# Kernel tuning notes

Measured on AMD Instinct MI355X. Metric: run time of the kernel, lower is better.

The kernel has to match this reference:

```python
import jax, jax.numpy as jnp
import numpy as np

B, C, D_MODEL, N_HEADS = 2, 2048, 1024, 16


def rotary_matrix(context_length: int, d: int) -> jnp.ndarray:
    """Faithful vectorization of get_rotary_matrix: theta = 10000^(-2*(i-1)/d)."""
    half = d // 2
    i = jnp.arange(half, dtype=jnp.float32)
    theta = 10000.0 ** (-2.0 * (i - 1.0) / d)          # note the (i-1), as in source
    m = jnp.arange(context_length, dtype=jnp.float32)
    ang = m[:, None] * theta                            # [C, d/2]
    c, s = jnp.cos(ang), jnp.sin(ang)
    ev = 2 * jnp.arange(half)
    od = ev + 1
    R = jnp.zeros((context_length, d, d), jnp.float32)
    R = R.at[:, ev, ev].set(c)
    R = R.at[:, ev, od].set(-s)
    R = R.at[:, od, ev].set(s)
    R = R.at[:, od, od].set(c)
    return R


def setup_inputs() -> dict:
    key = jax.random.key(0)
    k1, k2, k3, k4 = jax.random.split(key, 4)
    x = jax.random.normal(k1, (B, C, D_MODEL), dtype=jnp.float32)
    w_qkv = jax.random.normal(k2, (3 * D_MODEL, D_MODEL), dtype=jnp.float32) * 0.02
    w_out = jax.random.normal(k3, (D_MODEL, D_MODEL), dtype=jnp.float32) * 0.02
    b_out = jax.random.normal(k4, (D_MODEL,), dtype=jnp.float32) * 0.02
    return {"x": x, "w_qkv": w_qkv, "w_out": w_out, "b_out": b_out}


def reference(x, w_qkv, w_out, b_out):
    b, c, d = x.shape
    h = N_HEADS
    dh = d // h
    qkv = x @ w_qkv.T                                   # [B,C,3D]
    q, k, v = jnp.split(qkv, 3, axis=-1)
    # [B,C,D] -> [B,H,C,dh]
    q = q.reshape(b, c, h, dh).transpose(0, 2, 1, 3)
    k = k.reshape(b, c, h, dh).transpose(0, 2, 1, 3)
    v = v.reshape(b, c, h, dh).transpose(0, 2, 1, 3)
    R = rotary_matrix(c, dh)                            # [C,dh,dh]
    q_rot = jnp.einsum('bhci,cij->bhcj', q, R)
    k_rot = jnp.einsum('bhci,cij->bhcj', k, R)
    scale = jnp.sqrt(jnp.float32(dh))
    # exact math of the source: exp with no max subtraction, separate num/den
    attn_num = jnp.exp(jnp.einsum('bhqd,bhkd->bhqk', q_rot, k_rot) / scale)
    attn_den = jnp.exp(jnp.einsum('bhqd,bhkd->bhqk', q, k) / scale)
    attn_den = jnp.sum(attn_den, axis=-1, keepdims=True)
    attn = attn_num / attn_den
    causal = jnp.tril(jnp.ones((c, c), jnp.float32))[None, None]
    attn = jnp.where(causal == 0, 0.0, attn)
    y = jnp.einsum('bhqk,bhkd->bhqd', attn, v)
    y = y.transpose(0, 2, 1, 3).reshape(b, c, d)
    return y @ w_out.T + b_out
```

## Files before the change

### kernel.cpp

```cpp
#include <hip/hip_runtime.h>
#include <math.h>
#include <stdint.h>

#define BB 2
#define CC 2048
#define DD 1024
#define HH 16
#define DHH 64
#define HALF 32

typedef __attribute__((ext_vector_type(8))) short bf16x8;
typedef __attribute__((ext_vector_type(4))) float f32x4;
typedef unsigned int u32;

#define EXPC 0.1803368801f

__device__ __forceinline__ ushort f2bf(float f) {
    uint32_t u = __builtin_bit_cast(uint32_t, f);
    u = (u + 0x7FFFu + ((u >> 16) & 1u)) >> 16;
    return (ushort)u;
}

__device__ __forceinline__ void gload16(const void* g, void* lds) {
    __builtin_amdgcn_global_load_lds(
        (const u32 __attribute__((address_space(1)))*)g,
        (u32 __attribute__((address_space(3)))*)lds, 16, 0, 0);
}

__global__ __launch_bounds__(256) void cast3_k(const float* __restrict__ x,
                                               const float* __restrict__ wq,
                                               const float* __restrict__ wo,
                                               ushort* __restrict__ xb,
                                               ushort* __restrict__ wqb,
                                               ushort* __restrict__ wob) {
    int id = blockIdx.x * 256 + threadIdx.x;
    const float* s;
    ushort* d;
    int off;
    if (id < 524288)       { s = x;  d = xb;  off = id; }
    else if (id < 917504)  { s = wq; d = wqb; off = id - 524288; }
    else                   { s = wo; d = wob; off = id - 917504; }
    float4 a = *reinterpret_cast<const float4*>(s + (size_t)off * 8);
    float4 b = *reinterpret_cast<const float4*>(s + (size_t)off * 8 + 4);
    bf16x8 o;
    o[0] = (short)f2bf(a.x); o[1] = (short)f2bf(a.y);
    o[2] = (short)f2bf(a.z); o[3] = (short)f2bf(a.w);
    o[4] = (short)f2bf(b.x); o[5] = (short)f2bf(b.y);
    o[6] = (short)f2bf(b.z); o[7] = (short)f2bf(b.w);
    *reinterpret_cast<bf16x8*>(d + (size_t)off * 8) = o;
}

__global__ __launch_bounds__(256) void rope_table_k(float* __restrict__ ct, float* __restrict__ st) {
    int idx = blockIdx.x * 256 + threadIdx.x;
    if (idx >= CC * HALF) return;
    int m = idx >> 5;
    int t = idx & 31;
    double theta_d = pow(10000.0, -2.0 * ((double)t - 1.0) / 64.0);
    float theta = (float)theta_d;
    float ang = (float)m * theta;
    ct[idx] = cosf(ang);
    st[idx] = sinf(ang);
}

__global__ __launch_bounds__(256) void qkv_gemm_mfma_k(const ushort* __restrict__ xb,
                                                       const ushort* __restrict__ wqb,
                                                       const float* __restrict__ ct,
                                                       const float* __restrict__ st,
                                                       ushort* __restrict__ q,
                                                       ushort* __restrict__ k,
                                                       ushort* __restrict__ qr,
                                                       ushort* __restrict__ kr,
                                                       ushort* __restrict__ vT3) {
    __shared__ ushort Al[128 * 64];
    __shared__ ushort Bl[128 * 64];
    const int tid = threadIdx.x;
    const int w = tid >> 6, l = tid & 63;
    const int l15 = l & 15, lg = l >> 4;
    const int wr = w >> 1, wc = w & 1;
    const int m0 = blockIdx.x * 128, n0 = blockIdx.y * 128;
    const int lrow = l >> 3, lch = l & 7;

    f32x4 acc[4][4];
#pragma unroll
    for (int i = 0; i < 4; i++)
#pragma unroll
        for (int j = 0; j < 4; j++) acc[i][j] = (f32x4){0.f, 0.f, 0.f, 0.f};

    for (int k0 = 0; k0 < 1024; k0 += 64) {
        __syncthreads();
#pragma unroll
        for (int c = 0; c < 4; c++) {
            int row = w * 32 + c * 8 + lrow;
            int gch = (lch ^ (row & 7)) * 8;
            gload16(xb + (size_t)(m0 + row) * 1024 + k0 + gch, &Al[(w * 32 + c * 8) * 64]);
            gload16(wqb + (size_t)(n0 + row) * 1024 + k0 + gch, &Bl[(w * 32 + c * 8) * 64]);
        }
        __syncthreads();
#pragma unroll
        for (int kk = 0; kk < 2; kk++) {
            bf16x8 a[4], b[4];
#pragma unroll
            for (int mt = 0; mt < 4; mt++) {
                int row = wr * 64 + mt * 16 + l15;
                a[mt] = *reinterpret_cast<const bf16x8*>(&Al[row * 64 + ((kk * 4 + lg) ^ (row & 7)) * 8]);
            }
#pragma unroll
            for (int nt = 0; nt < 4; nt++) {
                int row = wc * 64 + nt * 16 + l15;
                b[nt] = *reinterpret_cast<const bf16x8*>(&Bl[row * 64 + ((kk * 4 + lg) ^ (row & 7)) * 8]);
            }
#pragma unroll
            for (int mt = 0; mt < 4; mt++)
#pragma unroll
                for (int nt = 0; nt < 4; nt++)
                    acc[mt][nt] = __builtin_amdgcn_mfma_f32_16x16x32_bf16(a[mt], b[nt], acc[mt][nt], 0, 0, 0);
        }
    }
#pragma unroll
    for (int mt = 0; mt < 4; mt++)
#pragma unroll
        for (int nt = 0; nt < 4; nt++) {
            int n = n0 + wc * 64 + nt * 16 + l15;
            int part = n >> 10;
            int d = n & 1023;
            int h = d >> 6, dd = d & 63;
            int mbase = m0 + wr * 64 + mt * 16 + lg * 4;
            int bb = mbase >> 11, cpos = mbase & 2047;
            if (part == 2) {
                int kt = cpos >> 6, kcol = cpos & 63;
                ushort4 pk;
                pk.x = f2bf(acc[mt][nt][0]); pk.y = f2bf(acc[mt][nt][1]);
                pk.z = f2bf(acc[mt][nt][2]); pk.w = f2bf(acc[mt][nt][3]);
                size_t off = ((((size_t)(bb * HH + h)) * 32 + kt) * 64 + dd) * 64 + kcol;
                *reinterpret_cast<ushort4*>(vT3 + off) = pk;
            } else {
                ushort* dstu = (part == 0) ? q : k;
                ushort* dstr = (part == 0) ? qr : kr;
                const float sgn = (dd & 1) ? -1.f : 1.f;
                const int t = dd >> 1;
#pragma unroll
                for (int r = 0; r < 4; r++) {
                    float val = acc[mt][nt][r];
                    float par = __shfl_xor(val, 1, 64);
                    float c = ct[(cpos + r) * 32 + t];
                    float s = st[(cpos + r) * 32 + t];
                    float rot = val * c + sgn * par * s;
                    size_t base = (((size_t)bb * HH + h) * CC + (cpos + r)) * DHH + dd;
                    dstu[base] = f2bf(val);
                    dstr[base] = f2bf(rot);
                }
            }
        }
}

__global__ __launch_bounds__(256, 2) void attn_fused_k(const ushort* __restrict__ vT3,
                                                       const ushort* __restrict__ qg,
                                                       const ushort* __restrict__ kg,
                                                       const ushort* __restrict__ qrg,
                                                       const ushort* __restrict__ krg,
                                                       ushort* __restrict__ y) {
    __shared__ ushort Kl[2][64 * 64];
    __shared__ ushort Krl[2][64 * 64];
    __shared__ ushort Pl[4][16 * 64];

    const int tid = threadIdx.x;
    const int w = tid >> 6, l = tid & 63;
    const int l15 = l & 15, lg = l >> 4;
    const int lrow = l >> 3, lch = l & 7;

    const int bid = blockIdx.x;
    const int xcd = bid & 7;
    const int idx = bid >> 3;
    const int sub = idx & 3;
    const int tp = idx >> 2;
    const int bh = xcd * 4 + sub;
    const int NB = 31 - tp;
    const int q0a = tp * 64;
    const int q0b = NB * 64;

    const ushort* qb  = qg  + (size_t)bh * CC * DHH;
    const ushort* kb  = kg  + (size_t)bh * CC * DHH;
    const ushort* qrb = qrg + (size_t)bh * CC * DHH;
    const ushort* krb = krg + (size_t)bh * CC * DHH;
    const ushort* vtb = vT3 + (size_t)bh * 32 * 64 * 64;

    bf16x8 qfA[2], qfB[2], qrfA[2], qrfB[2];
#pragma unroll
    for (int kk = 0; kk < 2; kk++) {
        int ra = q0a + w * 16 + l15;
        int rb = q0b + w * 16 + l15;
        qfA[kk]  = *reinterpret_cast<const bf16x8*>(qb  + (size_t)ra * DHH + kk * 32 + lg * 8);
        qfB[kk]  = *reinterpret_cast<const bf16x8*>(qb  + (size_t)rb * DHH + kk * 32 + lg * 8);
        qrfA[kk] = *reinterpret_cast<const bf16x8*>(qrb + (size_t)ra * DHH + kk * 32 + lg * 8);
        qrfB[kk] = *reinterpret_cast<const bf16x8*>(qrb + (size_t)rb * DHH + kk * 32 + lg * 8);
    }

    f32x4 yaccA[4], yaccB[4];
#pragma unroll
    for (int nt = 0; nt < 4; nt++) {
        yaccA[nt] = (f32x4){0.f, 0.f, 0.f, 0.f};
        yaccB[nt] = (f32x4){0.f, 0.f, 0.f, 0.f};
    }
    float daccA0 = 0.f, daccA1 = 0.f, daccB0 = 0.f, daccB1 = 0.f;

#define STAGE(KT, BUF)                                                                         \
    {                                                                                          \
        const int sk0 = (KT) * 64;                                                             \
        _Pragma("unroll")                                                                      \
        for (int c = 0; c < 2; c++) {                                                          \
            int row = w * 16 + c * 8 + lrow;                                                   \
            int gch = (lch ^ (row & 7)) * 8;                                                   \
            gload16(kb + (size_t)(sk0 + row) * DHH + gch, &Kl[BUF][(w * 16 + c * 8) * 64]);    \
            if ((KT) <= NB)                                                                    \
                gload16(krb + (size_t)(sk0 + row) * DHH + gch, &Krl[BUF][(w * 16 + c * 8) * 64]); \
        }                                                                                      \
    }

#define NUMPV(Q0, QRF, YACC, LASTKT)                                                           \
    {                                                                                          \
        const bool diag = (kt == (LASTKT));                                                    \
        const int qrow = (Q0) + w * 16 + l15;                                                  \
        _Pragma("unroll")                                                                      \
        for (int nt = 0; nt < 4; nt++) {                                                       \
            bf16x8 kra0, kra1;                                                                 \
            {                                                                                  \
                int krow = nt * 16 + l15;                                                      \
                kra0 = *reinterpret_cast<const bf16x8*>(&Krl[cur][krow * 64 + ((0 + lg) ^ (krow & 7)) * 8]); \
                kra1 = *reinterpret_cast<const bf16x8*>(&Krl[cur][krow * 64 + ((4 + lg) ^ (krow & 7)) * 8]); \
            }                                                                                  \
            __builtin_amdgcn_s_setprio(1);                                                     \
            f32x4 s = (f32x4){0.f, 0.f, 0.f, 0.f};                                             \
            s = __builtin_amdgcn_mfma_f32_16x16x32_bf16(kra0, (QRF)[0], s, 0, 0, 0);           \
            s = __builtin_amdgcn_mfma_f32_16x16x32_bf16(kra1, (QRF)[1], s, 0, 0, 0);           \
            __builtin_amdgcn_s_setprio(0);                                                     \
            float pe[4];                                                                       \
            _Pragma("unroll")                                                                  \
            for (int r = 0; r < 4; r++)                                                        \
                pe[r] = __builtin_amdgcn_exp2f(s[r] * EXPC);                                   \
            if (diag) {                                                                        \
                _Pragma("unroll")                                                              \
                for (int r = 0; r < 4; r++) {                                                  \
                    int key = kt * 64 + nt * 16 + lg * 4 + r;                                  \
                    pe[r] = (key <= qrow) ? pe[r] : 0.f;                                       \
                }                                                                              \
            }                                                                                  \
            u32 pk0, pk1;                                                                      \
            asm("v_cvt_pk_bf16_f32 %0, %1, %2" : "=v"(pk0) : "v"(pe[0]), "v"(pe[1]));          \
            asm("v_cvt_pk_bf16_f32 %0, %1, %2" : "=v"(pk1) : "v"(pe[2]), "v"(pe[3]));          \
            int swzc = (nt * 2 + (lg >> 1)) ^ (l15 & 7);                                       \
            uint2 pr; pr.x = pk0; pr.y = pk1;                                                  \
            *reinterpret_cast<uint2*>(&Pl[w][l15 * 64 + swzc * 8 + (lg & 1) * 4]) = pr;        \
        }                                                                                      \
        bf16x8 pa[2];                                                                          \
        _Pragma("unroll")                                                                      \
        for (int kk2 = 0; kk2 < 2; kk2++) {                                                    \
            int rc = (kk2 * 4 + lg) ^ (l15 & 7);                                               \
            pa[kk2] = *reinterpret_cast<const bf16x8*>(&Pl[w][l15 * 64 + rc * 8]);             \
        }                                                                                      \
        __builtin_amdgcn_s_setprio(1);                                                         \
        _Pragma("unroll")                                                                      \
        for (int nt2 = 0; nt2 < 4; nt2++) {                                                    \
            (YACC)[nt2] = __builtin_amdgcn_mfma_f32_16x16x32_bf16(pa[0], vf[nt2][0], (YACC)[nt2], 0, 0, 0); \
            (YACC)[nt2] = __builtin_amdgcn_mfma_f32_16x16x32_bf16(pa[1], vf[nt2][1], (YACC)[nt2], 0, 0, 0); \
        }                                                                                      \
        __builtin_amdgcn_s_setprio(0);                                                         \
    }

    STAGE(0, 0);
    __syncthreads();
    int cur = 0;

    for (int kt = 0; kt < 32; kt++) {
        const bool actA = (kt <= tp);
        const bool actB = (kt <= NB);

        bf16x8 vf[4][2];
        if (actB) {
            const ushort* vt0 = vtb + (size_t)kt * 64 * 64;
#pragma unroll
            for (int nt2 = 0; nt2 < 4; nt2++)
#pragma unroll
                for (int kk2 = 0; kk2 < 2; kk2++)
                    vf[nt2][kk2] = *reinterpret_cast<const bf16x8*>(
                        vt0 + (nt2 * 16 + l15) * 64 + kk2 * 32 + lg * 8);
        }

        if (kt + 1 < 32) STAGE(kt + 1, cur ^ 1);

#pragma unroll
        for (int nt = 0; nt < 4; nt++) {
            bf16x8 ka0, ka1;
            {
                int krow = nt * 16 + l15;
                ka0 = *reinterpret_cast<const bf16x8*>(&Kl[cur][krow * 64 + ((0 + lg) ^ (krow & 7)) * 8]);
                ka1 = *reinterpret_cast<const bf16x8*>(&Kl[cur][krow * 64 + ((4 + lg) ^ (krow & 7)) * 8]);
            }
            __builtin_amdgcn_s_setprio(1);
            f32x4 sA = (f32x4){0.f, 0.f, 0.f, 0.f};
            sA = __builtin_amdgcn_mfma_f32_16x16x32_bf16(ka0, qfA[0], sA, 0, 0, 0);
            sA = __builtin_amdgcn_mfma_f32_16x16x32_bf16(ka1, qfA[1], sA, 0, 0, 0);
            f32x4 sB = (f32x4){0.f, 0.f, 0.f, 0.f};
            sB = __builtin_amdgcn_mfma_f32_16x16x32_bf16(ka0, qfB[0], sB, 0, 0, 0);
            sB = __builtin_amdgcn_mfma_f32_16x16x32_bf16(ka1, qfB[1], sB, 0, 0, 0);
            __builtin_amdgcn_s_setprio(0);
            if (nt & 1) {
#pragma unroll
                for (int r = 0; r < 4; r++) {
                    daccA1 += __builtin_amdgcn_exp2f(sA[r] * EXPC);
                    daccB1 += __builtin_amdgcn_exp2f(sB[r] * EXPC);
                }
            } else {
#pragma unroll
                for (int r = 0; r < 4; r++) {
                    daccA0 += __builtin_amdgcn_exp2f(sA[r] * EXPC);
                    daccB0 += __builtin_amdgcn_exp2f(sB[r] * EXPC);
                }
            }
        }

        if (actB) NUMPV(q0b, qrfB, yaccB, NB);
        if (actA) NUMPV(q0a, qrfA, yaccA, tp);

        __syncthreads();
        cur ^= 1;
    }

    float denA = daccA0 + daccA1, denB = daccB0 + daccB1;
    denA += __shfl_xor(denA, 16, 64);
    denA += __shfl_xor(denA, 32, 64);
    denB += __shfl_xor(denB, 16, 64);
    denB += __shfl_xor(denB, 32, 64);

    const int b = bh >> 4, h = bh & 15;
#pragma unroll
    for (int r = 0; r < 4; r++) {
        float drA = __shfl(denA, lg * 4 + r, 64);
        float drB = __shfl(denB, lg * 4 + r, 64);
        float invA = 1.f / drA;
        float invB = 1.f / drB;
        int rowA = q0a + w * 16 + lg * 4 + r;
        int rowB = q0b + w * 16 + lg * 4 + r;
#pragma unroll
        for (int nt2 = 0; nt2 < 4; nt2++) {
            y[((size_t)b * CC + rowA) * DD + h * DHH + nt2 * 16 + l15] = f2bf(yaccA[nt2][r] * invA);
            y[((size_t)b * CC + rowB) * DD + h * DHH + nt2 * 16 + l15] = f2bf(yaccB[nt2][r] * invB);
        }
    }
#undef STAGE
#undef NUMPV
}

__global__ __launch_bounds__(256) void out_proj_mfma_k(const ushort* __restrict__ yb,
                                                       const ushort* __restrict__ wob,
                                                       const float* __restrict__ bias,
                                                       float* __restrict__ out) {
    __shared__ ushort Al[128 * 64];
    __shared__ ushort Bl[128 * 64];
    const int tid = threadIdx.x;
    const int w = tid >> 6, l = tid & 63;
    const int l15 = l & 15, lg = l >> 4;
    const int wr = w >> 1, wc = w & 1;
    const int m0 = blockIdx.x * 128, n0 = blockIdx.y * 128;
    const int lrow = l >> 3, lch = l & 7;

    f32x4 acc[4][4];
#pragma unroll
    for (int i = 0; i < 4; i++)
#pragma unroll
        for (int j = 0; j < 4; j++) acc[i][j] = (f32x4){0.f, 0.f, 0.f, 0.f};

    for (int k0 = 0; k0 < 1024; k0 += 64) {
        __syncthreads();
#pragma unroll
        for (int c = 0; c < 4; c++) {
            int row = w * 32 + c * 8 + lrow;
            int gch = (lch ^ (row & 7)) * 8;
            gload16(yb + (size_t)(m0 + row) * 1024 + k0 + gch, &Al[(w * 32 + c * 8) * 64]);
            gload16(wob + (size_t)(n0 + row) * 1024 + k0 + gch, &Bl[(w * 32 + c * 8) * 64]);
        }
        __syncthreads();
#pragma unroll
        for (int kk = 0; kk < 2; kk++) {
            bf16x8 a[4], b[4];
#pragma unroll
            for (int mt = 0; mt < 4; mt++) {
                int row = wr * 64 + mt * 16 + l15;
                a[mt] = *reinterpret_cast<const bf16x8*>(&Al[row * 64 + ((kk * 4 + lg) ^ (row & 7)) * 8]);
            }
#pragma unroll
            for (int nt = 0; nt < 4; nt++) {
                int row = wc * 64 + nt * 16 + l15;
                b[nt] = *reinterpret_cast<const bf16x8*>(&Bl[row * 64 + ((kk * 4 + lg) ^ (row & 7)) * 8]);
            }
#pragma unroll
            for (int mt = 0; mt < 4; mt++)
#pragma unroll
                for (int nt = 0; nt < 4; nt++)
                    acc[mt][nt] = __builtin_amdgcn_mfma_f32_16x16x32_bf16(a[mt], b[nt], acc[mt][nt], 0, 0, 0);
        }
    }
#pragma unroll
    for (int mt = 0; mt < 4; mt++)
#pragma unroll
        for (int nt = 0; nt < 4; nt++) {
            int n = n0 + wc * 64 + nt * 16 + l15;
            float bv = bias[n];
#pragma unroll
            for (int r = 0; r < 4; r++) {
                int m = m0 + wr * 64 + mt * 16 + lg * 4 + r;
                out[(size_t)m * 1024 + n] = acc[mt][nt][r] + bv;
            }
        }
}

extern "C" void kernel_launch(void* const* d_in, const int* in_sizes, int n_in,
                              void* d_out, int out_size, void* d_ws, size_t ws_size,
                              hipStream_t stream) {
    (void)in_sizes; (void)n_in; (void)out_size; (void)ws_size;
    const float* x     = (const float*)d_in[0];
    const float* w_qkv = (const float*)d_in[1];
    const float* w_out = (const float*)d_in[2];
    const float* b_out = (const float*)d_in[3];
    float* out = (float*)d_out;

    char* p = (char*)d_ws;
    float* ct = (float*)p;  p += (size_t)CC * HALF * 4;
    float* st = (float*)p;  p += (size_t)CC * HALF * 4;
    ushort* xb  = (ushort*)p; p += (size_t)4096 * 1024 * 2;
    ushort* wqb = (ushort*)p; p += (size_t)3072 * 1024 * 2;
    ushort* wob = (ushort*)p; p += (size_t)1024 * 1024 * 2;
    const size_t TEN = (size_t)BB * HH * CC * DHH;
    ushort* qb = (ushort*)p; p += TEN * 2;
    ushort* kb = (ushort*)p; p += TEN * 2;
    ushort* vT = (ushort*)p; p += TEN * 2;
    ushort* qr = (ushort*)p; p += TEN * 2;
    ushort* kr = (ushort*)p; p += TEN * 2;
    ushort* yb = (ushort*)p; p += (size_t)4096 * 1024 * 2;

    cast3_k<<<dim3(4096), dim3(256), 0, stream>>>(x, w_qkv, w_out, xb, wqb, wob);
    rope_table_k<<<dim3((CC * HALF) / 256), dim3(256), 0, stream>>>(ct, st);
    qkv_gemm_mfma_k<<<dim3(32, 24), dim3(256), 0, stream>>>(xb, wqb, ct, st, qb, kb, qr, kr, vT);
    attn_fused_k<<<dim3(512), dim3(256), 0, stream>>>(vT, qb, kb, qr, kr, yb);
    out_proj_mfma_k<<<dim3(32, 8), dim3(256), 0, stream>>>(yb, wob, b_out, out);
}
```

Baseline: 159.8 us.

## Widen attention key tile to 128 and fuse rope table into cast kernel

```diff
diff --git a/kernel.cpp b/kernel.cpp
--- a/kernel.cpp
+++ b/kernel.cpp
@@ -27,12 +27,25 @@
         (u32 __attribute__((address_space(3)))*)lds, 16, 0, 0);
 }
 
-__global__ __launch_bounds__(256) void cast3_k(const float* __restrict__ x,
-                                               const float* __restrict__ wq,
-                                               const float* __restrict__ wo,
-                                               ushort* __restrict__ xb,
-                                               ushort* __restrict__ wqb,
-                                               ushort* __restrict__ wob) {
+__global__ __launch_bounds__(256) void cast3_rope_k(const float* __restrict__ x,
+                                                    const float* __restrict__ wq,
+                                                    const float* __restrict__ wo,
+                                                    ushort* __restrict__ xb,
+                                                    ushort* __restrict__ wqb,
+                                                    ushort* __restrict__ wob,
+                                                    float* __restrict__ ct,
+                                                    float* __restrict__ st) {
+    if (blockIdx.x >= 4096) {
+        int idx = (blockIdx.x - 4096) * 256 + threadIdx.x;
+        int m = idx >> 5;
+        int t = idx & 31;
+        double theta_d = pow(10000.0, -2.0 * ((double)t - 1.0) / 64.0);
+        float theta = (float)theta_d;
+        float ang = (float)m * theta;
+        ct[idx] = cosf(ang);
+        st[idx] = sinf(ang);
+        return;
+    }
     int id = blockIdx.x * 256 + threadIdx.x;
     const float* s;
     ushort* d;
@@ -48,18 +61,6 @@
     o[4] = (short)f2bf(b.x); o[5] = (short)f2bf(b.y);
     o[6] = (short)f2bf(b.z); o[7] = (short)f2bf(b.w);
     *reinterpret_cast<bf16x8*>(d + (size_t)off * 8) = o;
-}
-
-__global__ __launch_bounds__(256) void rope_table_k(float* __restrict__ ct, float* __restrict__ st) {
-    int idx = blockIdx.x * 256 + threadIdx.x;
-    if (idx >= CC * HALF) return;
-    int m = idx >> 5;
-    int t = idx & 31;
-    double theta_d = pow(10000.0, -2.0 * ((double)t - 1.0) / 64.0);
-    float theta = (float)theta_d;
-    float ang = (float)m * theta;
-    ct[idx] = cosf(ang);
-    st[idx] = sinf(ang);
 }
 
 __global__ __launch_bounds__(256) void qkv_gemm_mfma_k(const ushort* __restrict__ xb,
@@ -159,9 +160,9 @@
                                                        const ushort* __restrict__ qrg,
                                                        const ushort* __restrict__ krg,
                                                        ushort* __restrict__ y) {
-    __shared__ ushort Kl[2][64 * 64];
-    __shared__ ushort Krl[2][64 * 64];
-    __shared__ ushort Pl[4][16 * 64];
+    __shared__ ushort Kl[2][128 * 64];
+    __shared__ ushort Krl[2][128 * 64];
+    __shared__ ushort Pl[4][16 * 128];
 
     const int tid = threadIdx.x;
     const int w = tid >> 6, l = tid & 63;
@@ -177,6 +178,8 @@
     const int NB = 31 - tp;
     const int q0a = tp * 64;
     const int q0b = NB * 64;
+    const int lastA = (q0a + 63) >> 7;
+    const int lastB = (q0b + 63) >> 7;
 
     const ushort* qb  = qg  + (size_t)bh * CC * DHH;
     const ushort* kb  = kg  + (size_t)bh * CC * DHH;
@@ -205,23 +208,23 @@
 
 #define STAGE(KT, BUF)                                                                         \
     {                                                                                          \
-        const int sk0 = (KT) * 64;                                                             \
+        const int sk0 = (KT) * 128;                                                            \
         _Pragma("unroll")                                                                      \
-        for (int c = 0; c < 2; c++) {                                                          \
-            int row = w * 16 + c * 8 + lrow;                                                   \
+        for (int c = 0; c < 4; c++) {                                                          \
+            int row = w * 32 + c * 8 + lrow;                                                   \
             int gch = (lch ^ (row & 7)) * 8;                                                   \
-            gload16(kb + (size_t)(sk0 + row) * DHH + gch, &Kl[BUF][(w * 16 + c * 8) * 64]);    \
-            if ((KT) <= NB)                                                                    \
-                gload16(krb + (size_t)(sk0 + row) * DHH + gch, &Krl[BUF][(w * 16 + c * 8) * 64]); \
+            gload16(kb + (size_t)(sk0 + row) * DHH + gch, &Kl[BUF][(w * 32 + c * 8) * 64]);    \
+            if ((KT) <= lastB)                                                                 \
+                gload16(krb + (size_t)(sk0 + row) * DHH + gch, &Krl[BUF][(w * 32 + c * 8) * 64]); \
         }                                                                                      \
     }
 
-#define NUMPV(Q0, QRF, YACC, LASTKT)                                                           \
+#define NUMPV(Q0, QRF, YACC, LASTT)                                                            \
     {                                                                                          \
-        const bool diag = (kt == (LASTKT));                                                    \
+        const bool diag = (kt == (LASTT));                                                     \
         const int qrow = (Q0) + w * 16 + l15;                                                  \
         _Pragma("unroll")                                                                      \
-        for (int nt = 0; nt < 4; nt++) {                                                       \
+        for (int nt = 0; nt < 8; nt++) {                                                       \
             bf16x8 kra0, kra1;                                                                 \
             {                                                                                  \
                 int krow = nt * 16 + l15;                                                      \
@@ -240,7 +243,7 @@
             if (diag) {                                                                        \
                 _Pragma("unroll")                                                              \
                 for (int r = 0; r < 4; r++) {                                                  \
-                    int key = kt * 64 + nt * 16 + lg * 4 + r;                                  \
+                    int key = kt * 128 + nt * 16 + lg * 4 + r;                                 \
                     pe[r] = (key <= qrow) ? pe[r] : 0.f;                                       \
                 }                                                                              \
             }                                                                                  \
@@ -249,19 +252,21 @@
             asm("v_cvt_pk_bf16_f32 %0, %1, %2" : "=v"(pk1) : "v"(pe[2]), "v"(pe[3]));          \
             int swzc = (nt * 2 + (lg >> 1)) ^ (l15 & 7);                                       \
             uint2 pr; pr.x = pk0; pr.y = pk1;                                                  \
-            *reinterpret_cast<uint2*>(&Pl[w][l15 * 64 + swzc * 8 + (lg & 1) * 4]) = pr;        \
+            *reinterpret_cast<uint2*>(&Pl[w][l15 * 128 + swzc * 8 + (lg & 1) * 4]) = pr;       \
         }                                                                                      \
-        bf16x8 pa[2];                                                                          \
+        bf16x8 pa[4];                                                                          \
         _Pragma("unroll")                                                                      \
-        for (int kk2 = 0; kk2 < 2; kk2++) {                                                    \
+        for (int kk2 = 0; kk2 < 4; kk2++) {                                                    \
             int rc = (kk2 * 4 + lg) ^ (l15 & 7);                                               \
-            pa[kk2] = *reinterpret_cast<const bf16x8*>(&Pl[w][l15 * 64 + rc * 8]);             \
+            pa[kk2] = *reinterpret_cast<const bf16x8*>(&Pl[w][l15 * 128 + rc * 8]);            \
         }                                                                                      \
         __builtin_amdgcn_s_setprio(1);                                                         \
         _Pragma("unroll")                                                                      \
         for (int nt2 = 0; nt2 < 4; nt2++) {                                                    \
             (YACC)[nt2] = __builtin_amdgcn_mfma_f32_16x16x32_bf16(pa[0], vf[nt2][0], (YACC)[nt2], 0, 0, 0); \
             (YACC)[nt2] = __builtin_amdgcn_mfma_f32_16x16x32_bf16(pa[1], vf[nt2][1], (YACC)[nt2], 0, 0, 0); \
+            (YACC)[nt2] = __builtin_amdgcn_mfma_f32_16x16x32_bf16(pa[2], vf[nt2][2], (YACC)[nt2], 0, 0, 0); \
+            (YACC)[nt2] = __builtin_amdgcn_mfma_f32_16x16x32_bf16(pa[3], vf[nt2][3], (YACC)[nt2], 0, 0, 0); \
         }                                                                                      \
         __builtin_amdgcn_s_setprio(0);                                                         \
     }
@@ -270,25 +275,27 @@
     __syncthreads();
     int cur = 0;
 
-    for (int kt = 0; kt < 32; kt++) {
-        const bool actA = (kt <= tp);
-        const bool actB = (kt <= NB);
-
-        bf16x8 vf[4][2];
+    for (int kt = 0; kt < 16; kt++) {
+        const bool actA = (kt <= lastA);
+        const bool actB = (kt <= lastB);
+
+        bf16x8 vf[4][4];
         if (actB) {
-            const ushort* vt0 = vtb + (size_t)kt * 64 * 64;
-#pragma unroll
-            for (int nt2 = 0; nt2 < 4; nt2++)
-#pragma unroll
-                for (int kk2 = 0; kk2 < 2; kk2++)
-                    vf[nt2][kk2] = *reinterpret_cast<const bf16x8*>(
-                        vt0 + (nt2 * 16 + l15) * 64 + kk2 * 32 + lg * 8);
-        }
-
-        if (kt + 1 < 32) STAGE(kt + 1, cur ^ 1);
-
-#pragma unroll
-        for (int nt = 0; nt < 4; nt++) {
+            const ushort* vt0 = vtb + (size_t)(2 * kt) * 64 * 64;
+            const ushort* vt1 = vt0 + 64 * 64;
+#pragma unroll
+            for (int nt2 = 0; nt2 < 4; nt2++) {
+                vf[nt2][0] = *reinterpret_cast<const bf16x8*>(vt0 + (nt2 * 16 + l15) * 64 + lg * 8);
+                vf[nt2][1] = *reinterpret_cast<const bf16x8*>(vt0 + (nt2 * 16 + l15) * 64 + 32 + lg * 8);
+                vf[nt2][2] = *reinterpret_cast<const bf16x8*>(vt1 + (nt2 * 16 + l15) * 64 + lg * 8);
+                vf[nt2][3] = *reinterpret_cast<const bf16x8*>(vt1 + (nt2 * 16 + l15) * 64 + 32 + lg * 8);
+            }
+        }
+
+        if (kt + 1 < 16) STAGE(kt + 1, cur ^ 1);
+
+#pragma unroll
+        for (int nt = 0; nt < 8; nt++) {
             bf16x8 ka0, ka1;
             {
                 int krow = nt * 16 + l15;
@@ -318,8 +325,8 @@
             }
         }
 
-        if (actB) NUMPV(q0b, qrfB, yaccB, NB);
-        if (actA) NUMPV(q0a, qrfA, yaccA, tp);
+        if (actB) NUMPV(q0b, qrfB, yaccB, lastB);
+        if (actA) NUMPV(q0a, qrfA, yaccA, lastA);
 
         __syncthreads();
         cur ^= 1;
@@ -437,8 +444,7 @@
     ushort* kr = (ushort*)p; p += TEN * 2;
     ushort* yb = (ushort*)p; p += (size_t)4096 * 1024 * 2;
 
-    cast3_k<<<dim3(4096), dim3(256), 0, stream>>>(x, w_qkv, w_out, xb, wqb, wob);
-    rope_table_k<<<dim3((CC * HALF) / 256), dim3(256), 0, stream>>>(ct, st);
+    cast3_rope_k<<<dim3(4352), dim3(256), 0, stream>>>(x, w_qkv, w_out, xb, wqb, wob, ct, st);
     qkv_gemm_mfma_k<<<dim3(32, 24), dim3(256), 0, stream>>>(xb, wqb, ct, st, qb, kb, qr, kr, vT);
     attn_fused_k<<<dim3(512), dim3(256), 0, stream>>>(vT, qb, kb, qr, kr, yb);
     out_proj_mfma_k<<<dim3(32, 8), dim3(256), 0, stream>>>(yb, wob, b_out, out);
```

Result: no change. 157.5 us (-1.4%).
